# Performance work log

Measured on AMD Instinct MI355X. Metric: run time of the kernel, lower is better.

The kernel has to match this reference:

```python
import jax, jax.numpy as jnp
import numpy as np

PATCH = 16
EPS = 1e-5


def _conv_offsets(x, offset_w, offset_b):
    # offset conv: same kernel/stride/padding as the deform conv
    off = jax.lax.conv_general_dilated(
        x, offset_w, window_strides=(PATCH, PATCH), padding='VALID',
        dimension_numbers=('NCHW', 'OIHW', 'NCHW'))
    return off + offset_b[None, :, None, None]


def _deform_conv(x, offset_w, offset_b, dconv_w):
    B, C, H, W = x.shape
    kh = kw = PATCH
    K = kh * kw
    Ho, Wo = H // PATCH, W // PATCH

    off = _conv_offsets(x, offset_w, offset_b)            # [B, 2K, Ho, Wo]
    # mmcv layout: channels are (dy, dx) pairs per kernel point
    off = off.reshape(B, K, 2, Ho, Wo)
    dy = off[:, :, 0].transpose(0, 2, 3, 1)               # [B, Ho, Wo, K]
    dx = off[:, :, 1].transpose(0, 2, 3, 1)

    ii, jj = jnp.meshgrid(jnp.arange(kh), jnp.arange(kw), indexing='ij')
    ki = ii.reshape(-1).astype(x.dtype)                   # [K]
    kj = jj.reshape(-1).astype(x.dtype)
    base_y = (jnp.arange(Ho, dtype=x.dtype) * PATCH)[:, None] + ki[None, :]  # [Ho, K]
    base_x = (jnp.arange(Wo, dtype=x.dtype) * PATCH)[:, None] + kj[None, :]  # [Wo, K]

    py = base_y[None, :, None, :] + dy                    # [B, Ho, Wo, K]
    px = base_x[None, None, :, :] + dx

    y0 = jnp.floor(py); x0 = jnp.floor(px)
    wy1 = py - y0; wx1 = px - x0
    wy0 = 1.0 - wy1; wx0 = 1.0 - wx1
    y0i = y0.astype(jnp.int32); x0i = x0.astype(jnp.int32)
    y1i = y0i + 1;              x1i = x0i + 1

    xt = x.transpose(0, 2, 3, 1)                          # [B, H, W, C]
    bidx = jnp.arange(B)[:, None, None, None]

    def gather(yi, xi):
        ok = ((yi >= 0) & (yi < H) & (xi >= 0) & (xi < W)).astype(x.dtype)
        v = xt[bidx, jnp.clip(yi, 0, H - 1), jnp.clip(xi, 0, W - 1)]  # [B,Ho,Wo,K,C]
        return v * ok[..., None]

    sampled = (gather(y0i, x0i) * (wy0 * wx0)[..., None]
               + gather(y0i, x1i) * (wy0 * wx1)[..., None]
               + gather(y1i, x0i) * (wy1 * wx0)[..., None]
               + gather(y1i, x1i) * (wy1 * wx1)[..., None])  # [B,Ho,Wo,K,C]

    Wk = dconv_w.reshape(dconv_w.shape[0], C, K)          # [O, C, K]
    out = jnp.einsum('bhwkc,ock->bohw', sampled, Wk)      # [B, O, Ho, Wo]
    return out


def setup_inputs() -> dict:
    key = jax.random.key(0)
    ks = jax.random.split(key, 3)
    B, C, H, W = 64, 3, 224, 224
    O = 768
    x = jax.random.normal(ks[0], (B, C, H, W), jnp.float32)
    # small offset weights -> offsets of O(1) pixel, exercising bilinear path
    offset_w = jax.random.normal(ks[1], (2 * PATCH * PATCH, C, PATCH, PATCH), jnp.float32) * 0.01
    offset_b = jnp.zeros((2 * PATCH * PATCH,), jnp.float32)
    dconv_w = jax.random.normal(ks[2], (O, C, PATCH, PATCH), jnp.float32) * 0.02
    bn_gamma = jnp.ones((O,), jnp.float32)
    bn_beta = jnp.zeros((O,), jnp.float32)
    return {"x": x, "offset_w": offset_w, "offset_b": offset_b,
            "dconv_w": dconv_w, "bn_gamma": bn_gamma, "bn_beta": bn_beta}


def reference(x, offset_w, offset_b, dconv_w, bn_gamma, bn_beta):
    B = x.shape[0]
    y = _deform_conv(x, offset_w, offset_b, dconv_w)      # [B, O, Ho, Wo]
    # BatchNorm2d (training-mode batch stats, biased var) per torch semantics
    mean = jnp.mean(y, axis=(0, 2, 3), keepdims=True)
    var = jnp.mean((y - mean) ** 2, axis=(0, 2, 3), keepdims=True)
    yn = (y - mean) * jax.lax.rsqrt(var + EPS)
    yn = yn * bn_gamma[None, :, None, None] + bn_beta[None, :, None, None]
    ya = jax.nn.gelu(yn, approximate=False)               # nn.GELU default = exact
    O, Ho, Wo = ya.shape[1], ya.shape[2], ya.shape[3]
    return ya.reshape(B, O, Ho * Wo).transpose(0, 2, 1)   # [B, N, embed_dim]
```

## Files before the change

kernel.cpp:

```cpp
#include <hip/hip_runtime.h>
#include <math.h>

#define PATCH 16
#define BATCH 64
#define CIN 3
#define HH 224
#define WW 224
#define NPATCH (BATCH*14*14)
#define KDIM 768
#define NOFF 512
#define NOUT 768
#define KPTS 256
#define EPSF 1e-5f
#define CHW (CIN*HH*WW)
#define HWX (HH*WW)
#define NRB (NPATCH/128)

using short8 = __attribute__((ext_vector_type(8))) short;
using f32x4  = __attribute__((ext_vector_type(4))) float;

#define GLOAD16(g, l) __builtin_amdgcn_global_load_lds( \
    (const __attribute__((address_space(1))) void*)(g), \
    (__attribute__((address_space(3))) void*)(l), 16, 0, 0)

__device__ __forceinline__ unsigned short f2bf(float f) {
    unsigned int u = __float_as_uint(f);
    u = (u + 0x7fffu + ((u >> 16) & 1u)) >> 16;
    return (unsigned short)u;
}
__device__ __forceinline__ float bf2f(unsigned short h) {
    return __uint_as_float(((unsigned int)h) << 16);
}
__device__ __forceinline__ float gelu_exact(float v) {
    return 0.5f * v * (1.0f + erff(v * 0.70710678118654752440f));
}

#define N4X (BATCH*CHW/4)
#define N4W1 (NOFF*KDIM/4)
#define N4W2 (NOUT*KDIM/4)
#define N4ALL (N4X+N4W1+N4W2)

__global__ __launch_bounds__(256) void cvt_all(
    const float* __restrict__ x, const float* __restrict__ w1,
    const float* __restrict__ w2, unsigned short* __restrict__ xbf,
    unsigned short* __restrict__ wbf1, unsigned short* __restrict__ wbf2)
{
    for (int i = blockIdx.x*256 + threadIdx.x; i < N4ALL; i += gridDim.x*256) {
        const float* src; unsigned short* dst; int j;
        if (i < N4X)            { src = x;  dst = xbf;  j = i; }
        else if (i < N4X+N4W1)  { src = w1; dst = wbf1; j = i - N4X; }
        else                    { src = w2; dst = wbf2; j = i - N4X - N4W1; }
        float4 v = ((const float4*)src)[j];
        ((ushort4*)dst)[j] = make_ushort4(f2bf(v.x), f2bf(v.y), f2bf(v.z), f2bf(v.w));
    }
}

__global__ __launch_bounds__(256) void gemm_offsets(
    const unsigned short* __restrict__ xbf, const unsigned short* __restrict__ Bw,
    const float* __restrict__ offb, unsigned short* __restrict__ off)
{
    __shared__ unsigned short lds[4*8192];
    const int t = threadIdx.x;
    const int lane = t & 63;
    const int w = t >> 6, wr = w >> 1, wc = w & 1;

    int bid = blockIdx.x;
    int idx = (bid & 7)*49 + (bid >> 3);
    const int bm = (idx >> 2) * 128, bn = (idx & 3) * 128;

    const int rq = t >> 2;
    const int ksw = (((t & 3) ^ ((t >> 3) & 3)) << 3);

    const unsigned short* aBase0;
    const unsigned short* aBase1;
    {
        int p0 = bm + rq,      b0 = p0/196, r0 = p0%196;
        int p1 = bm + 64 + rq, b1 = p1/196, r1 = p1%196;
        aBase0 = xbf + (size_t)b0*CHW + (size_t)((r0/14)*PATCH)*WW + (size_t)((r0%14)*PATCH);
        aBase1 = xbf + (size_t)b1*CHW + (size_t)((r1/14)*PATCH)*WW + (size_t)((r1%14)*PATCH);
    }
    const unsigned short* bS0 = Bw + (size_t)(bn + rq)*KDIM + ksw;
    const unsigned short* bS1 = Bw + (size_t)(bn + 64 + rq)*KDIM + ksw;

    const int row_a = wr*64 + (lane & 15);
    const int row_b = wc*64 + (lane & 15);
    const int klocs = (((lane >> 4) ^ ((lane >> 1) & 3)) << 3);

#define STG1(slot, k0) do { \
        unsigned short* d = lds + (slot)*8192 + t*8; \
        int e = (k0) + ksw; \
        size_t xo = (size_t)(e >> 8)*HWX + (size_t)((e >> 4) & 15)*WW + (e & 15); \
        GLOAD16(aBase0 + xo, d); \
        GLOAD16(aBase1 + xo, d + 2048); \
        GLOAD16(bS0 + (k0), d + 4096); \
        GLOAD16(bS1 + (k0), d + 6144); \
    } while(0)

    f32x4 acc[4][4] = {};
    STG1(0, 0); STG1(1, 32); STG1(2, 64);
    asm volatile("s_waitcnt vmcnt(8)" ::: "memory");
    __builtin_amdgcn_s_barrier();
#pragma unroll
    for (int it = 0; it < 24; ++it) {
        if (it + 3 < 24) STG1((it+3)&3, (it+3)*32);
        const unsigned short* As_ = lds + (it&3)*8192;
        const unsigned short* Bs_ = As_ + 4096;
        short8 af[4], bv[4];
#pragma unroll
        for (int m = 0; m < 4; ++m) af[m] = *(const short8*)&As_[(row_a + m*16)*32 + klocs];
#pragma unroll
        for (int n = 0; n < 4; ++n) bv[n] = *(const short8*)&Bs_[(row_b + n*16)*32 + klocs];
        __builtin_amdgcn_s_setprio(1);
#pragma unroll
        for (int m = 0; m < 4; ++m)
#pragma unroll
            for (int n = 0; n < 4; ++n)
                acc[m][n] = __builtin_amdgcn_mfma_f32_16x16x32_bf16(af[m], bv[n], acc[m][n], 0, 0, 0);
        __builtin_amdgcn_s_setprio(0);
        if (it <= 20)      { asm volatile("s_waitcnt vmcnt(8) lgkmcnt(0)" ::: "memory"); __builtin_amdgcn_s_barrier(); }
        else if (it == 21) { asm volatile("s_waitcnt vmcnt(4) lgkmcnt(0)" ::: "memory"); __builtin_amdgcn_s_barrier(); }
        else if (it == 22) { asm volatile("s_waitcnt vmcnt(0) lgkmcnt(0)" ::: "memory"); __builtin_amdgcn_s_barrier(); }
    }
#undef STG1

    const int col0 = bn + wc*64 + (lane & 15);
    const int r0 = (lane >> 4) * 4;
#pragma unroll
    for (int m = 0; m < 4; ++m) {
        int grow = bm + wr*64 + m*16 + r0;
#pragma unroll
        for (int n = 0; n < 4; ++n) {
            int gcol = col0 + n*16;
            float bias = offb[gcol];
#pragma unroll
            for (int r = 0; r < 4; ++r)
                off[(size_t)(grow + r)*NOFF + gcol] = f2bf(acc[m][n][r] + bias);
        }
    }
}

__global__ __launch_bounds__(256) void sampler(
    const unsigned short* __restrict__ xbf, const unsigned int* __restrict__ offu,
    unsigned short* __restrict__ A2)
{
    __shared__ unsigned short win[3][22][24];
    int p = blockIdx.x;
    int k = threadIdx.x;
    int b = p / 196, rem = p % 196;
    int ho = rem / 14, wo = rem % 14;
    const int gy0 = ho*PATCH - 2, gx0 = wo*PATCH - 2;
    const unsigned short* xb = xbf + (size_t)b*CHW;

    bool interior = (ho >= 1) && (ho <= 12) && (wo >= 1) && (wo <= 12);
    if (interior) {
        for (int idx = k; idx < 3*22*11; idx += 256) {
            int c = idx / 242, r2 = idx - c*242;
            int row = r2 / 11, u = r2 - row*11;
            const unsigned int* src = (const unsigned int*)
                (xb + (size_t)c*HWX + (size_t)(gy0+row)*WW + gx0);
            *(unsigned int*)&win[c][row][2*u] = src[u];
        }
    } else {
        for (int idx = k; idx < 3*22*22; idx += 256) {
            int c = idx / 484, r2 = idx - c*484;
            int row = r2 / 22, col = r2 - row*22;
            int gy = min(max(gy0+row, 0), HH-1);
            int gx = min(max(gx0+col, 0), WW-1);
            win[c][row][col] = xb[(size_t)c*HWX + (size_t)gy*WW + gx];
        }
    }
    __syncthreads();

    unsigned int d2 = offu[(size_t)p*KPTS + k];
    float dy = __uint_as_float((d2 & 0xffffu) << 16);
    float dx = __uint_as_float(d2 & 0xffff0000u);
    float py = (float)(ho*PATCH + (k >> 4)) + dy;
    float px = (float)(wo*PATCH + (k & 15)) + dx;
    float fy = floorf(py), fx = floorf(px);
    float wy1 = py - fy, wx1 = px - fx;
    float wy0 = 1.f - wy1, wx0 = 1.f - wx1;
    int y0 = (int)fy, x0 = (int)fx;
    int y1 = y0 + 1, x1 = x0 + 1;
    bool oky0 = (y0 >= 0) & (y0 < HH);
    bool oky1 = (y1 >= 0) & (y1 < HH);
    bool okx0 = (x0 >= 0) & (x0 < WW);
    bool okx1 = (x1 >= 0) & (x1 < WW);
    float w00 = wy0*wx0, w01 = wy0*wx1, w10 = wy1*wx0, w11 = wy1*wx1;

    int ry = y0 - gy0, rx = x0 - gx0;
    if (ry >= 0 && ry <= 20 && rx >= 0 && rx <= 20) {
        float m00 = oky0 && okx0 ? 1.f : 0.f;
        float m01 = oky0 && okx1 ? 1.f : 0.f;
        float m10 = oky1 && okx0 ? 1.f : 0.f;
        float m11 = oky1 && okx1 ? 1.f : 0.f;
#pragma unroll
        for (int c = 0; c < CIN; ++c) {
            float v00 = bf2f(win[c][ry  ][rx  ]) * m00;
            float v01 = bf2f(win[c][ry  ][rx+1]) * m01;
            float v10 = bf2f(win[c][ry+1][rx  ]) * m10;
            float v11 = bf2f(win[c][ry+1][rx+1]) * m11;
            float v = v00*w00 + v01*w01 + v10*w10 + v11*w11;
            A2[(size_t)p*KDIM + c*KPTS + k] = f2bf(v);
        }
    } else {
        int yc0 = min(max(y0, 0), HH-1), yc1 = min(max(y1, 0), HH-1);
        int xc0 = min(max(x0, 0), WW-1), xc1 = min(max(x1, 0), WW-1);
#pragma unroll
        for (int c = 0; c < CIN; ++c) {
            const unsigned short* xc = xb + (size_t)c*HWX;
            float v00 = (oky0 && okx0) ? bf2f(xc[(size_t)yc0*WW + xc0]) : 0.f;
            float v01 = (oky0 && okx1) ? bf2f(xc[(size_t)yc0*WW + xc1]) : 0.f;
            float v10 = (oky1 && okx0) ? bf2f(xc[(size_t)yc1*WW + xc0]) : 0.f;
            float v11 = (oky1 && okx1) ? bf2f(xc[(size_t)yc1*WW + xc1]) : 0.f;
            float v = v00*w00 + v01*w01 + v10*w10 + v11*w11;
            A2[(size_t)p*KDIM + c*KPTS + k] = f2bf(v);
        }
    }
}

__global__ __launch_bounds__(512) void gemm_deform(
    const unsigned short* __restrict__ A, const unsigned short* __restrict__ Bw,
    unsigned short* __restrict__ Cbf, float* __restrict__ psum, float* __restrict__ psq)
{
    __shared__ unsigned short lds[3*12288];
    __shared__ float redS[2][256];
    __shared__ float redQ[2][256];
    const int t = threadIdx.x;
    const int lane = t & 63;
    const int w = t >> 6;
    const int wr = w >> 2, wc = w & 3;

    int bid = blockIdx.x;
    int xcd = bid & 7, j = bid >> 3;
    int idx = (xcd < 6) ? xcd*37 + j : 222 + (xcd-6)*36 + j;
    const int rblk = idx / 3;
    const int bm = rblk*128, bn = (idx % 3)*256;

    const int rq = t >> 2;
    const int ksw = (((t & 3) ^ ((t >> 3) & 3)) << 3);

    const unsigned short* aS  = A  + (size_t)(bm + rq)*KDIM + ksw;
    const unsigned short* bS0 = Bw + (size_t)(bn + rq)*KDIM + ksw;
    const unsigned short* bS1 = Bw + (size_t)(bn + 128 + rq)*KDIM + ksw;

    const int row_a = wr*64 + (lane & 15);
    const int row_b = wc*64 + (lane & 15);
    const int klocs = (((lane >> 4) ^ ((lane >> 1) & 3)) << 3);

#define STG(slot, k0) do { \
        unsigned short* d = lds + (slot)*12288 + t*8; \
        GLOAD16(aS  + (k0), d);           \
        GLOAD16(bS0 + (k0), d + 4096);    \
        GLOAD16(bS1 + (k0), d + 8192);    \
    } while(0)

    f32x4 acc[4][4] = {};
    STG(0, 0); STG(1, 32);
    asm volatile("s_waitcnt vmcnt(3)" ::: "memory");
    __builtin_amdgcn_s_barrier();
#pragma unroll
    for (int it = 0; it < 24; ++it) {
        if (it + 2 < 24) STG((it+2)%3, (it+2)*32);
        const unsigned short* As_ = lds + (it%3)*12288;
        const unsigned short* Bs_ = As_ + 4096;
        short8 af[4], bv[4];
#pragma unroll
        for (int m = 0; m < 4; ++m) af[m] = *(const short8*)&As_[(row_a + m*16)*32 + klocs];
#pragma unroll
        for (int n = 0; n < 4; ++n) bv[n] = *(const short8*)&Bs_[(row_b + n*16)*32 + klocs];
        __builtin_amdgcn_s_setprio(1);
#pragma unroll
        for (int m = 0; m < 4; ++m)
#pragma unroll
            for (int n = 0; n < 4; ++n)
                acc[m][n] = __builtin_amdgcn_mfma_f32_16x16x32_bf16(af[m], bv[n], acc[m][n], 0, 0, 0);
        __builtin_amdgcn_s_setprio(0);
        if (it < 22)       { asm volatile("s_waitcnt vmcnt(3) lgkmcnt(0)" ::: "memory"); __builtin_amdgcn_s_barrier(); }
        else if (it == 22) { asm volatile("s_waitcnt vmcnt(0) lgkmcnt(0)" ::: "memory"); __builtin_amdgcn_s_barrier(); }
    }
#undef STG

    float s[4] = {}, q[4] = {};
#pragma unroll
    for (int m = 0; m < 4; ++m)
#pragma unroll
        for (int n = 0; n < 4; ++n)
#pragma unroll
            for (int r = 0; r < 4; ++r) {
                float v = acc[m][n][r];
                s[n] += v; q[n] += v*v;
            }
#pragma unroll
    for (int n = 0; n < 4; ++n) {
        s[n] += __shfl_xor(s[n], 16); q[n] += __shfl_xor(q[n], 16);
        s[n] += __shfl_xor(s[n], 32); q[n] += __shfl_xor(q[n], 32);
    }
    if (lane < 16) {
#pragma unroll
        for (int n = 0; n < 4; ++n) {
            redS[wr][wc*64 + n*16 + lane] = s[n];
            redQ[wr][wc*64 + n*16 + lane] = q[n];
        }
    }
    __syncthreads();

    const int col0 = bn + wc*64 + (lane & 15);
    const int r0 = (lane >> 4) * 4;
#pragma unroll
    for (int m = 0; m < 4; ++m) {
        int grow = bm + wr*64 + m*16 + r0;
#pragma unroll
        for (int n = 0; n < 4; ++n) {
            int gcol = col0 + n*16;
#pragma unroll
            for (int r = 0; r < 4; ++r)
                Cbf[(size_t)(grow + r)*NOUT + gcol] = f2bf(acc[m][n][r]);
        }
    }
    if (t < 256) {
        psum[(size_t)rblk*NOUT + bn + t] = redS[0][t] + redS[1][t];
        psq [(size_t)rblk*NOUT + bn + t] = redQ[0][t] + redQ[1][t];
    }
}

__global__ __launch_bounds__(256) void bn_final(
    const float* __restrict__ psum, const float* __restrict__ psq,
    const float* __restrict__ gamma, const float* __restrict__ beta,
    float* __restrict__ scale, float* __restrict__ shift)
{
    int o = blockIdx.x*256 + threadIdx.x;
    float s = 0.f, q = 0.f;
    for (int i = 0; i < NRB; ++i) {
        s += psum[(size_t)i*NOUT + o];
        q += psq [(size_t)i*NOUT + o];
    }
    float mean = s * (1.0f/(float)NPATCH);
    float var  = q * (1.0f/(float)NPATCH) - mean*mean;
    float inv  = 1.0f / sqrtf(var + EPSF);
    float sc   = gamma[o] * inv;
    scale[o] = sc;
    shift[o] = beta[o] - mean*sc;
}

__global__ __launch_bounds__(256) void norm_gelu(
    const unsigned short* __restrict__ ybf, float* __restrict__ out,
    const float* __restrict__ scale, const float* __restrict__ shift)
{
    __shared__ float ssc[NOUT], ssh[NOUT];
    for (int i = threadIdx.x; i < NOUT; i += 256) { ssc[i] = scale[i]; ssh[i] = shift[i]; }
    __syncthreads();
    const size_t total8 = (size_t)NPATCH * NOUT / 8;
    for (size_t i = (size_t)blockIdx.x*256 + threadIdx.x; i < total8;
         i += (size_t)gridDim.x*256) {
        uint4 v = ((const uint4*)ybf)[i];
        int og = (int)(i % (NOUT/8)) * 8;
        float4 o0, o1;
        o0.x = gelu_exact(__uint_as_float(v.x << 16)        * ssc[og+0] + ssh[og+0]);
        o0.y = gelu_exact(__uint_as_float(v.x & 0xffff0000u)* ssc[og+1] + ssh[og+1]);
        o0.z = gelu_exact(__uint_as_float(v.y << 16)        * ssc[og+2] + ssh[og+2]);
        o0.w = gelu_exact(__uint_as_float(v.y & 0xffff0000u)* ssc[og+3] + ssh[og+3]);
        o1.x = gelu_exact(__uint_as_float(v.z << 16)        * ssc[og+4] + ssh[og+4]);
        o1.y = gelu_exact(__uint_as_float(v.z & 0xffff0000u)* ssc[og+5] + ssh[og+5]);
        o1.z = gelu_exact(__uint_as_float(v.w << 16)        * ssc[og+6] + ssh[og+6]);
        o1.w = gelu_exact(__uint_as_float(v.w & 0xffff0000u)* ssc[og+7] + ssh[og+7]);
        ((float4*)out)[2*i]   = o0;
        ((float4*)out)[2*i+1] = o1;
    }
}

extern "C" void kernel_launch(void* const* d_in, const int* in_sizes, int n_in,
                              void* d_out, int out_size, void* d_ws, size_t ws_size,
                              hipStream_t stream)
{
    const float* x      = (const float*)d_in[0];
    const float* offw   = (const float*)d_in[1];
    const float* offb   = (const float*)d_in[2];
    const float* dconvw = (const float*)d_in[3];
    const float* gamma  = (const float*)d_in[4];
    const float* beta   = (const float*)d_in[5];
    float* out = (float*)d_out;

    const size_t NX  = (size_t)BATCH*CHW;
    const size_t NW1 = (size_t)NOFF*KDIM;
    const size_t NW2 = (size_t)NOUT*KDIM;

    unsigned short* xbf   = (unsigned short*)d_ws;
    unsigned short* wbf1  = xbf  + NX;
    unsigned short* wbf2  = wbf1 + NW1;
    unsigned short* A2    = wbf2 + NW2;
    unsigned short* off   = A2   + (size_t)NPATCH*KDIM;
    unsigned short* ybf   = off  + (size_t)NPATCH*NOFF;
    float* fscratch = (float*)(ybf + (size_t)NPATCH*NOUT);
    float* psum  = fscratch;
    float* psq   = psum + NRB*NOUT;
    float* scale = psq  + NRB*NOUT;
    float* shift = scale + NOUT;

    cvt_all<<<4096, 256, 0, stream>>>(x, offw, dconvw, xbf, wbf1, wbf2);
    gemm_offsets<<<392, 256, 0, stream>>>(xbf, wbf1, offb, off);
    sampler<<<NPATCH, 256, 0, stream>>>(xbf, (const unsigned int*)off, A2);
    gemm_deform<<<294, 512, 0, stream>>>(A2, wbf2, ybf, psum, psq);
    bn_final<<<3, 256, 0, stream>>>(psum, psq, gamma, beta, scale, shift);
    norm_gelu<<<2048, 256, 0, stream>>>(ybf, out, scale, shift);
}
```

Baseline: 110.3 us.

## Fuse input bf16 conversion into offset GEMM and read fp32 input in sampler

Drops the standalone pass that converted the whole input image to bf16. The offset GEMM now loads fp32 image rows into registers, packs them to bf16 and writes them to LDS itself, with the pipeline cut from four stages to three. The sampler reads the fp32 input directly into an fp32 LDS window. This removes a full read and write of the input, in exchange for register-staged A loads in the GEMM that may hide latency less well than the previous direct global-to-LDS copies.

```diff
diff --git a/kernel.cpp b/kernel.cpp
--- a/kernel.cpp
+++ b/kernel.cpp
@@ -28,38 +28,38 @@
     u = (u + 0x7fffu + ((u >> 16) & 1u)) >> 16;
     return (unsigned short)u;
 }
-__device__ __forceinline__ float bf2f(unsigned short h) {
-    return __uint_as_float(((unsigned int)h) << 16);
-}
 __device__ __forceinline__ float gelu_exact(float v) {
     return 0.5f * v * (1.0f + erff(v * 0.70710678118654752440f));
 }
-
-#define N4X (BATCH*CHW/4)
+__device__ __forceinline__ short8 pack8(float4 u, float4 v) {
+    short8 r;
+    r[0]=(short)f2bf(u.x); r[1]=(short)f2bf(u.y); r[2]=(short)f2bf(u.z); r[3]=(short)f2bf(u.w);
+    r[4]=(short)f2bf(v.x); r[5]=(short)f2bf(v.y); r[6]=(short)f2bf(v.z); r[7]=(short)f2bf(v.w);
+    return r;
+}
+
 #define N4W1 (NOFF*KDIM/4)
 #define N4W2 (NOUT*KDIM/4)
-#define N4ALL (N4X+N4W1+N4W2)
-
-__global__ __launch_bounds__(256) void cvt_all(
-    const float* __restrict__ x, const float* __restrict__ w1,
-    const float* __restrict__ w2, unsigned short* __restrict__ xbf,
+#define N4W  (N4W1+N4W2)
+
+__global__ __launch_bounds__(256) void cvt_w(
+    const float* __restrict__ w1, const float* __restrict__ w2,
     unsigned short* __restrict__ wbf1, unsigned short* __restrict__ wbf2)
 {
-    for (int i = blockIdx.x*256 + threadIdx.x; i < N4ALL; i += gridDim.x*256) {
-        const float* src; unsigned short* dst; int j;
-        if (i < N4X)            { src = x;  dst = xbf;  j = i; }
-        else if (i < N4X+N4W1)  { src = w1; dst = wbf1; j = i - N4X; }
-        else                    { src = w2; dst = wbf2; j = i - N4X - N4W1; }
-        float4 v = ((const float4*)src)[j];
-        ((ushort4*)dst)[j] = make_ushort4(f2bf(v.x), f2bf(v.y), f2bf(v.z), f2bf(v.w));
-    }
+    int i = blockIdx.x*256 + threadIdx.x;
+    if (i >= N4W) return;
+    const float* src; unsigned short* dst; int j;
+    if (i < N4W1) { src = w1; dst = wbf1; j = i; }
+    else          { src = w2; dst = wbf2; j = i - N4W1; }
+    float4 v = ((const float4*)src)[j];
+    ((ushort4*)dst)[j] = make_ushort4(f2bf(v.x), f2bf(v.y), f2bf(v.z), f2bf(v.w));
 }
 
 __global__ __launch_bounds__(256) void gemm_offsets(
-    const unsigned short* __restrict__ xbf, const unsigned short* __restrict__ Bw,
+    const float* __restrict__ x, const unsigned short* __restrict__ Bw,
     const float* __restrict__ offb, unsigned short* __restrict__ off)
 {
-    __shared__ unsigned short lds[4*8192];
+    __shared__ unsigned short lds[3*8192];
     const int t = threadIdx.x;
     const int lane = t & 63;
     const int w = t >> 6, wr = w >> 1, wc = w & 1;
@@ -71,13 +71,12 @@
     const int rq = t >> 2;
     const int ksw = (((t & 3) ^ ((t >> 3) & 3)) << 3);
 
-    const unsigned short* aBase0;
-    const unsigned short* aBase1;
+    const float* aF0; const float* aF1;
     {
         int p0 = bm + rq,      b0 = p0/196, r0 = p0%196;
         int p1 = bm + 64 + rq, b1 = p1/196, r1 = p1%196;
-        aBase0 = xbf + (size_t)b0*CHW + (size_t)((r0/14)*PATCH)*WW + (size_t)((r0%14)*PATCH);
-        aBase1 = xbf + (size_t)b1*CHW + (size_t)((r1/14)*PATCH)*WW + (size_t)((r1%14)*PATCH);
+        aF0 = x + (size_t)b0*CHW + (size_t)((r0/14)*PATCH)*WW + (size_t)((r0%14)*PATCH);
+        aF1 = x + (size_t)b1*CHW + (size_t)((r1/14)*PATCH)*WW + (size_t)((r1%14)*PATCH);
     }
     const unsigned short* bS0 = Bw + (size_t)(bn + rq)*KDIM + ksw;
     const unsigned short* bS1 = Bw + (size_t)(bn + 64 + rq)*KDIM + ksw;
@@ -86,24 +85,32 @@
     const int row_b = wc*64 + (lane & 15);
     const int klocs = (((lane >> 4) ^ ((lane >> 1) & 3)) << 3);
 
-#define STG1(slot, k0) do { \
-        unsigned short* d = lds + (slot)*8192 + t*8; \
-        int e = (k0) + ksw; \
+    float4 a0, a1, a2, a3;
+#define LOADA(k0) do { int e = (k0) + ksw; \
         size_t xo = (size_t)(e >> 8)*HWX + (size_t)((e >> 4) & 15)*WW + (e & 15); \
-        GLOAD16(aBase0 + xo, d); \
-        GLOAD16(aBase1 + xo, d + 2048); \
-        GLOAD16(bS0 + (k0), d + 4096); \
-        GLOAD16(bS1 + (k0), d + 6144); \
-    } while(0)
+        a0 = *(const float4*)(aF0 + xo); a1 = *(const float4*)(aF0 + xo + 4); \
+        a2 = *(const float4*)(aF1 + xo); a3 = *(const float4*)(aF1 + xo + 4); } while(0)
+#define GLB(slot, k0) do { unsigned short* d = lds + (slot)*8192 + t*8; \
+        GLOAD16(bS0 + (k0), d + 4096); GLOAD16(bS1 + (k0), d + 6144); } while(0)
+#define WRITEA(slot) do { unsigned short* d = lds + (slot)*8192 + t*8; \
+        *(short8*)d = pack8(a0, a1); *(short8*)(d + 2048) = pack8(a2, a3); } while(0)
 
     f32x4 acc[4][4] = {};
-    STG1(0, 0); STG1(1, 32); STG1(2, 64);
+    LOADA(0); GLB(0, 0);
+    float4 b0_ = a0, b1_ = a1, b2_ = a2, b3_ = a3;
+    LOADA(32); GLB(1, 32);
     asm volatile("s_waitcnt vmcnt(8)" ::: "memory");
+    { unsigned short* d = lds + t*8;
+      *(short8*)d = pack8(b0_, b1_); *(short8*)(d + 2048) = pack8(b2_, b3_); }
+    asm volatile("s_waitcnt vmcnt(2)" ::: "memory");
+    WRITEA(1);
+    asm volatile("s_waitcnt lgkmcnt(0)" ::: "memory");
     __builtin_amdgcn_s_barrier();
+
 #pragma unroll
     for (int it = 0; it < 24; ++it) {
-        if (it + 3 < 24) STG1((it+3)&3, (it+3)*32);
-        const unsigned short* As_ = lds + (it&3)*8192;
+        if (it + 2 < 24) { LOADA((it+2)*32); GLB((it+2)%3, (it+2)*32); }
+        const unsigned short* As_ = lds + (it%3)*8192;
         const unsigned short* Bs_ = As_ + 4096;
         short8 af[4], bv[4];
 #pragma unroll
@@ -117,11 +124,19 @@
             for (int n = 0; n < 4; ++n)
                 acc[m][n] = __builtin_amdgcn_mfma_f32_16x16x32_bf16(af[m], bv[n], acc[m][n], 0, 0, 0);
         __builtin_amdgcn_s_setprio(0);
-        if (it <= 20)      { asm volatile("s_waitcnt vmcnt(8) lgkmcnt(0)" ::: "memory"); __builtin_amdgcn_s_barrier(); }
-        else if (it == 21) { asm volatile("s_waitcnt vmcnt(4) lgkmcnt(0)" ::: "memory"); __builtin_amdgcn_s_barrier(); }
-        else if (it == 22) { asm volatile("s_waitcnt vmcnt(0) lgkmcnt(0)" ::: "memory"); __builtin_amdgcn_s_barrier(); }
-    }
-#undef STG1
+        if (it + 2 < 24) {
+            asm volatile("s_waitcnt vmcnt(2)" ::: "memory");
+            WRITEA((it+2)%3);
+            asm volatile("s_waitcnt lgkmcnt(0)" ::: "memory");
+            __builtin_amdgcn_s_barrier();
+        } else if (it == 22) {
+            asm volatile("s_waitcnt vmcnt(0) lgkmcnt(0)" ::: "memory");
+            __builtin_amdgcn_s_barrier();
+        }
+    }
+#undef LOADA
+#undef GLB
+#undef WRITEA
 
     const int col0 = bn + wc*64 + (lane & 15);
     const int r0 = (lane >> 4) * 4;
@@ -140,25 +155,24 @@
 }
 
 __global__ __launch_bounds__(256) void sampler(
-    const unsigned short* __restrict__ xbf, const unsigned int* __restrict__ offu,
+    const float* __restrict__ x, const unsigned int* __restrict__ offu,
     unsigned short* __restrict__ A2)
 {
-    __shared__ unsigned short win[3][22][24];
+    __shared__ float win[3][22][24];
     int p = blockIdx.x;
     int k = threadIdx.x;
     int b = p / 196, rem = p % 196;
     int ho = rem / 14, wo = rem % 14;
     const int gy0 = ho*PATCH - 2, gx0 = wo*PATCH - 2;
-    const unsigned short* xb = xbf + (size_t)b*CHW;
+    const float* xb = x + (size_t)b*CHW;
 
     bool interior = (ho >= 1) && (ho <= 12) && (wo >= 1) && (wo <= 12);
     if (interior) {
         for (int idx = k; idx < 3*22*11; idx += 256) {
             int c = idx / 242, r2 = idx - c*242;
             int row = r2 / 11, u = r2 - row*11;
-            const unsigned int* src = (const unsigned int*)
-                (xb + (size_t)c*HWX + (size_t)(gy0+row)*WW + gx0);
-            *(unsigned int*)&win[c][row][2*u] = src[u];
+            float2 s = *(const float2*)(xb + (size_t)c*HWX + (size_t)(gy0+row)*WW + gx0 + 2*u);
+            *(float2*)&win[c][row][2*u] = s;
         }
     } else {
         for (int idx = k; idx < 3*22*22; idx += 256) {
@@ -195,11 +209,10 @@
         float m11 = oky1 && okx1 ? 1.f : 0.f;
 #pragma unroll
         for (int c = 0; c < CIN; ++c) {
-            float v00 = bf2f(win[c][ry  ][rx  ]) * m00;
-            float v01 = bf2f(win[c][ry  ][rx+1]) * m01;
-            float v10 = bf2f(win[c][ry+1][rx  ]) * m10;
-            float v11 = bf2f(win[c][ry+1][rx+1]) * m11;
-            float v = v00*w00 + v01*w01 + v10*w10 + v11*w11;
+            float v = win[c][ry  ][rx  ] * m00 * w00
+                    + win[c][ry  ][rx+1] * m01 * w01
+                    + win[c][ry+1][rx  ] * m10 * w10
+                    + win[c][ry+1][rx+1] * m11 * w11;
             A2[(size_t)p*KDIM + c*KPTS + k] = f2bf(v);
         }
     } else {
@@ -207,11 +220,11 @@
         int xc0 = min(max(x0, 0), WW-1), xc1 = min(max(x1, 0), WW-1);
 #pragma unroll
         for (int c = 0; c < CIN; ++c) {
-            const unsigned short* xc = xb + (size_t)c*HWX;
-            float v00 = (oky0 && okx0) ? bf2f(xc[(size_t)yc0*WW + xc0]) : 0.f;
-            float v01 = (oky0 && okx1) ? bf2f(xc[(size_t)yc0*WW + xc1]) : 0.f;
-            float v10 = (oky1 && okx0) ? bf2f(xc[(size_t)yc1*WW + xc0]) : 0.f;
-            float v11 = (oky1 && okx1) ? bf2f(xc[(size_t)yc1*WW + xc1]) : 0.f;
+            const float* xc = xb + (size_t)c*HWX;
+            float v00 = (oky0 && okx0) ? xc[(size_t)yc0*WW + xc0] : 0.f;
+            float v01 = (oky0 && okx1) ? xc[(size_t)yc0*WW + xc1] : 0.f;
+            float v10 = (oky1 && okx0) ? xc[(size_t)yc1*WW + xc0] : 0.f;
+            float v11 = (oky1 && okx1) ? xc[(size_t)yc1*WW + xc1] : 0.f;
             float v = v00*w00 + v01*w01 + v10*w10 + v11*w11;
             A2[(size_t)p*KDIM + c*KPTS + k] = f2bf(v);
         }
@@ -249,9 +262,9 @@
 
 #define STG(slot, k0) do { \
         unsigned short* d = lds + (slot)*12288 + t*8; \
-        GLOAD16(aS  + (k0), d);           \
-        GLOAD16(bS0 + (k0), d + 4096);    \
-        GLOAD16(bS1 + (k0), d + 8192);    \
+        GLOAD16(aS  + (k0), d); \
+        GLOAD16(bS0 + (k0), d + 4096); \
+        GLOAD16(bS1 + (k0), d + 8192); \
     } while(0)
 
     f32x4 acc[4][4] = {};
@@ -380,12 +393,10 @@
     const float* beta   = (const float*)d_in[5];
     float* out = (float*)d_out;
 
-    const size_t NX  = (size_t)BATCH*CHW;
     const size_t NW1 = (size_t)NOFF*KDIM;
     const size_t NW2 = (size_t)NOUT*KDIM;
 
-    unsigned short* xbf   = (unsigned short*)d_ws;
-    unsigned short* wbf1  = xbf  + NX;
+    unsigned short* wbf1  = (unsigned short*)d_ws;
     unsigned short* wbf2  = wbf1 + NW1;
     unsigned short* A2    = wbf2 + NW2;
     unsigned short* off   = A2   + (size_t)NPATCH*KDIM;
@@ -396,9 +407,9 @@
     float* scale = psq  + NRB*NOUT;
     float* shift = scale + NOUT;
 
-    cvt_all<<<4096, 256, 0, stream>>>(x, offw, dconvw, xbf, wbf1, wbf2);
-    gemm_offsets<<<392, 256, 0, stream>>>(xbf, wbf1, offb, off);
-    sampler<<<NPATCH, 256, 0, stream>>>(xbf, (const unsigned int*)off, A2);
+    cvt_w<<<(N4W + 255)/256, 256, 0, stream>>>(offw, dconvw, wbf1, wbf2);
+    gemm_offsets<<<392, 256, 0, stream>>>(x, wbf1, offb, off);
+    sampler<<<NPATCH, 256, 0, stream>>>(x, (const unsigned int*)off, A2);
     gemm_deform<<<294, 512, 0, stream>>>(A2, wbf2, ybf, psum, psq);
     bn_final<<<3, 256, 0, stream>>>(psum, psq, gamma, beta, scale, shift);
     norm_gelu<<<2048, 256, 0, stream>>>(ybf, out, scale, shift);
```

Result: slower. 123.2 us (+11.7%).

## Enlarge deform GEMM tile to 256x256 with four-stage split-phase LDS pipeline

Applied to the files above, without the earlier changes.

The deform-conv GEMM moves from 128x256 to 256x256 output tiles per block, halving the grid to 147 blocks, with each wave holding 8x4 accumulators. The K loop becomes a 4-slot LDS ring where A and B staging is split into separate phases, interleaved with half-width MFMA bursts and barriers (a ping-pong style schedule). This aims to raise operand reuse and hide global loads behind MFMA, at the cost of more registers, more barriers, and only 147 blocks on a 256-CU device, so many CUs sit idle. BN partial sums now reuse the staging LDS and each block writes two 128-row partials.

```diff
diff --git a/kernel.cpp b/kernel.cpp
--- a/kernel.cpp
+++ b/kernel.cpp
@@ -222,67 +222,129 @@
     const unsigned short* __restrict__ A, const unsigned short* __restrict__ Bw,
     unsigned short* __restrict__ Cbf, float* __restrict__ psum, float* __restrict__ psq)
 {
-    __shared__ unsigned short lds[3*12288];
-    __shared__ float redS[2][256];
-    __shared__ float redQ[2][256];
+    __shared__ unsigned short lds[4*16384];
     const int t = threadIdx.x;
     const int lane = t & 63;
     const int w = t >> 6;
     const int wr = w >> 2, wc = w & 3;
 
     int bid = blockIdx.x;
-    int xcd = bid & 7, j = bid >> 3;
-    int idx = (xcd < 6) ? xcd*37 + j : 222 + (xcd-6)*36 + j;
-    const int rblk = idx / 3;
-    const int bm = rblk*128, bn = (idx % 3)*256;
-
-    const int rq = t >> 2;
-    const int ksw = (((t & 3) ^ ((t >> 3) & 3)) << 3);
-
-    const unsigned short* aS  = A  + (size_t)(bm + rq)*KDIM + ksw;
-    const unsigned short* bS0 = Bw + (size_t)(bn + rq)*KDIM + ksw;
-    const unsigned short* bS1 = Bw + (size_t)(bn + 128 + rq)*KDIM + ksw;
-
-    const int row_a = wr*64 + (lane & 15);
-    const int row_b = wc*64 + (lane & 15);
+    int xcd = bid & 7, jj = bid >> 3;
+    int idx = (xcd < 3) ? xcd*19 + jj : 57 + (xcd-3)*18 + jj;
+    const int mblk = idx / 3;
+    const int bm = mblk*256, bn = (idx % 3)*256;
+
+    const int schunk = ((t & 3) ^ ((t >> 3) & 3)) << 3;
+    const unsigned short* aSrc = A  + (size_t)(bm + (t >> 2))*KDIM + schunk;
+    const unsigned short* bSrc = Bw + (size_t)(bn + (t >> 2))*KDIM + schunk;
+
+#define STG_A(s, k0) do { \
+        unsigned short* d = lds + (s)*16384 + t*8; \
+        GLOAD16(aSrc + (k0), d); \
+        GLOAD16(aSrc + (size_t)128*KDIM + (k0), d + 4096); } while(0)
+#define STG_B(s, k0) do { \
+        unsigned short* d = lds + (s)*16384 + 8192 + t*8; \
+        GLOAD16(bSrc + (k0), d); \
+        GLOAD16(bSrc + (size_t)128*KDIM + (k0), d + 4096); } while(0)
+
     const int klocs = (((lane >> 4) ^ ((lane >> 1) & 3)) << 3);
-
-#define STG(slot, k0) do { \
-        unsigned short* d = lds + (slot)*12288 + t*8; \
-        GLOAD16(aS  + (k0), d);           \
-        GLOAD16(bS0 + (k0), d + 4096);    \
-        GLOAD16(bS1 + (k0), d + 8192);    \
-    } while(0)
-
-    f32x4 acc[4][4] = {};
-    STG(0, 0); STG(1, 32);
-    asm volatile("s_waitcnt vmcnt(3)" ::: "memory");
+    const int arow0 = wr*128 + (lane & 15);
+    const int brow0 = wc*64  + (lane & 15);
+
+    f32x4 acc[8][4] = {};
+
+    STG_A(0, 0);  STG_B(0, 0);
+    STG_A(1, 32); STG_B(1, 32);
+    asm volatile("s_waitcnt vmcnt(4)" ::: "memory");
     __builtin_amdgcn_s_barrier();
-#pragma unroll
-    for (int it = 0; it < 24; ++it) {
-        if (it + 2 < 24) STG((it+2)%3, (it+2)*32);
-        const unsigned short* As_ = lds + (it%3)*12288;
-        const unsigned short* Bs_ = As_ + 4096;
-        short8 af[4], bv[4];
-#pragma unroll
-        for (int m = 0; m < 4; ++m) af[m] = *(const short8*)&As_[(row_a + m*16)*32 + klocs];
-#pragma unroll
-        for (int n = 0; n < 4; ++n) bv[n] = *(const short8*)&Bs_[(row_b + n*16)*32 + klocs];
+
+    short8 af[8], bv[4];
+    for (int kt = 0; kt < 12; ++kt) {
+        const int s0 = (2*kt) & 3;
+        const int s1 = s0 + 1;
+        const int s2 = (s0 + 2) & 3;
+        const int s3 = (s0 + 3) & 3;
+        const int k2 = (2*kt + 2) * 32;
+        const int k3 = (2*kt + 3) * 32;
+        const unsigned short* H0 = lds + s0*16384;
+        const unsigned short* H1 = lds + s1*16384;
+
+#pragma unroll
+        for (int m = 0; m < 8; ++m) af[m] = *(const short8*)&H0[(arow0 + m*16)*32 + klocs];
+        bv[0] = *(const short8*)&H0[8192 + (brow0 +  0)*32 + klocs];
+        bv[1] = *(const short8*)&H0[8192 + (brow0 + 16)*32 + klocs];
+        if (kt < 11) STG_A(s2, k2);
+        __builtin_amdgcn_s_barrier();
+        asm volatile("s_waitcnt lgkmcnt(0)" ::: "memory");
         __builtin_amdgcn_s_setprio(1);
 #pragma unroll
-        for (int m = 0; m < 4; ++m)
-#pragma unroll
-            for (int n = 0; n < 4; ++n)
-                acc[m][n] = __builtin_amdgcn_mfma_f32_16x16x32_bf16(af[m], bv[n], acc[m][n], 0, 0, 0);
+        for (int m = 0; m < 8; ++m) {
+            acc[m][0] = __builtin_amdgcn_mfma_f32_16x16x32_bf16(af[m], bv[0], acc[m][0], 0, 0, 0);
+            acc[m][1] = __builtin_amdgcn_mfma_f32_16x16x32_bf16(af[m], bv[1], acc[m][1], 0, 0, 0);
+        }
         __builtin_amdgcn_s_setprio(0);
-        if (it < 22)       { asm volatile("s_waitcnt vmcnt(3) lgkmcnt(0)" ::: "memory"); __builtin_amdgcn_s_barrier(); }
-        else if (it == 22) { asm volatile("s_waitcnt vmcnt(0) lgkmcnt(0)" ::: "memory"); __builtin_amdgcn_s_barrier(); }
-    }
-#undef STG
+        asm volatile("s_waitcnt lgkmcnt(0)" ::: "memory");
+        __builtin_amdgcn_s_barrier();
+
+        bv[2] = *(const short8*)&H0[8192 + (brow0 + 32)*32 + klocs];
+        bv[3] = *(const short8*)&H0[8192 + (brow0 + 48)*32 + klocs];
+        if (kt < 11) { STG_B(s2, k2);
+            asm volatile("s_waitcnt vmcnt(4)" ::: "memory");
+        } else {
+            asm volatile("s_waitcnt vmcnt(0)" ::: "memory");
+        }
+        __builtin_amdgcn_s_barrier();
+        asm volatile("s_waitcnt lgkmcnt(0)" ::: "memory");
+        __builtin_amdgcn_s_setprio(1);
+#pragma unroll
+        for (int m = 0; m < 8; ++m) {
+            acc[m][2] = __builtin_amdgcn_mfma_f32_16x16x32_bf16(af[m], bv[2], acc[m][2], 0, 0, 0);
+            acc[m][3] = __builtin_amdgcn_mfma_f32_16x16x32_bf16(af[m], bv[3], acc[m][3], 0, 0, 0);
+        }
+        __builtin_amdgcn_s_setprio(0);
+        asm volatile("s_waitcnt lgkmcnt(0)" ::: "memory");
+        __builtin_amdgcn_s_barrier();
+
+#pragma unroll
+        for (int m = 0; m < 8; ++m) af[m] = *(const short8*)&H1[(arow0 + m*16)*32 + klocs];
+        bv[0] = *(const short8*)&H1[8192 + (brow0 +  0)*32 + klocs];
+        bv[1] = *(const short8*)&H1[8192 + (brow0 + 16)*32 + klocs];
+        if (kt < 11) STG_A(s3, k3);
+        __builtin_amdgcn_s_barrier();
+        asm volatile("s_waitcnt lgkmcnt(0)" ::: "memory");
+        __builtin_amdgcn_s_setprio(1);
+#pragma unroll
+        for (int m = 0; m < 8; ++m) {
+            acc[m][0] = __builtin_amdgcn_mfma_f32_16x16x32_bf16(af[m], bv[0], acc[m][0], 0, 0, 0);
+            acc[m][1] = __builtin_amdgcn_mfma_f32_16x16x32_bf16(af[m], bv[1], acc[m][1], 0, 0, 0);
+        }
+        __builtin_amdgcn_s_setprio(0);
+        asm volatile("s_waitcnt lgkmcnt(0)" ::: "memory");
+        __builtin_amdgcn_s_barrier();
+
+        bv[2] = *(const short8*)&H1[8192 + (brow0 + 32)*32 + klocs];
+        bv[3] = *(const short8*)&H1[8192 + (brow0 + 48)*32 + klocs];
+        if (kt < 11) { STG_B(s3, k3);
+            asm volatile("s_waitcnt vmcnt(4)" ::: "memory");
+        }
+        __builtin_amdgcn_s_barrier();
+        asm volatile("s_waitcnt lgkmcnt(0)" ::: "memory");
+        __builtin_amdgcn_s_setprio(1);
+#pragma unroll
+        for (int m = 0; m < 8; ++m) {
+            acc[m][2] = __builtin_amdgcn_mfma_f32_16x16x32_bf16(af[m], bv[2], acc[m][2], 0, 0, 0);
+            acc[m][3] = __builtin_amdgcn_mfma_f32_16x16x32_bf16(af[m], bv[3], acc[m][3], 0, 0, 0);
+        }
+        __builtin_amdgcn_s_setprio(0);
+        asm volatile("s_waitcnt lgkmcnt(0)" ::: "memory");
+        __builtin_amdgcn_s_barrier();
+    }
+#undef STG_A
+#undef STG_B
 
     float s[4] = {}, q[4] = {};
 #pragma unroll
-    for (int m = 0; m < 4; ++m)
+    for (int m = 0; m < 8; ++m)
 #pragma unroll
         for (int n = 0; n < 4; ++n)
 #pragma unroll
@@ -295,11 +357,15 @@
         s[n] += __shfl_xor(s[n], 16); q[n] += __shfl_xor(q[n], 16);
         s[n] += __shfl_xor(s[n], 32); q[n] += __shfl_xor(q[n], 32);
     }
+
+    __syncthreads();
+    float* redS = (float*)lds;
+    float* redQ = redS + 512;
     if (lane < 16) {
 #pragma unroll
         for (int n = 0; n < 4; ++n) {
-            redS[wr][wc*64 + n*16 + lane] = s[n];
-            redQ[wr][wc*64 + n*16 + lane] = q[n];
+            redS[wr*256 + wc*64 + n*16 + lane] = s[n];
+            redQ[wr*256 + wc*64 + n*16 + lane] = q[n];
         }
     }
     __syncthreads();
@@ -307,8 +373,8 @@
     const int col0 = bn + wc*64 + (lane & 15);
     const int r0 = (lane >> 4) * 4;
 #pragma unroll
-    for (int m = 0; m < 4; ++m) {
-        int grow = bm + wr*64 + m*16 + r0;
+    for (int m = 0; m < 8; ++m) {
+        int grow = bm + wr*128 + m*16 + r0;
 #pragma unroll
         for (int n = 0; n < 4; ++n) {
             int gcol = col0 + n*16;
@@ -317,9 +383,11 @@
                 Cbf[(size_t)(grow + r)*NOUT + gcol] = f2bf(acc[m][n][r]);
         }
     }
-    if (t < 256) {
-        psum[(size_t)rblk*NOUT + bn + t] = redS[0][t] + redS[1][t];
-        psq [(size_t)rblk*NOUT + bn + t] = redQ[0][t] + redQ[1][t];
+    {
+        int half = t >> 8;
+        int c = t & 255;
+        psum[(size_t)(bm/128 + half)*NOUT + bn + c] = redS[half*256 + c];
+        psq [(size_t)(bm/128 + half)*NOUT + bn + c] = redQ[half*256 + c];
     }
 }
 
@@ -399,7 +467,7 @@
     cvt_all<<<4096, 256, 0, stream>>>(x, offw, dconvw, xbf, wbf1, wbf2);
     gemm_offsets<<<392, 256, 0, stream>>>(xbf, wbf1, offb, off);
     sampler<<<NPATCH, 256, 0, stream>>>(xbf, (const unsigned int*)off, A2);
-    gemm_deform<<<294, 512, 0, stream>>>(A2, wbf2, ybf, psum, psq);
+    gemm_deform<<<147, 512, 0, stream>>>(A2, wbf2, ybf, psum, psq);
     bn_final<<<3, 256, 0, stream>>>(psum, psq, gamma, beta, scale, shift);
     norm_gelu<<<2048, 256, 0, stream>>>(ybf, out, scale, shift);
 }
```

New measurement: 102.7 us. -6.9%, faster.
